# Performance work log

Hardware: AMD Instinct MI355X
Metric: run time of the kernel (lower is better)

Reference implementation:

```python
import jax, jax.numpy as jnp
import numpy as np
from jax import lax

B, N, C, H = 1024, 169, 256, 4   # n must equal window**2 = 169
A, W = 169, 13                   # agent_num, window; pool_size = sqrt(A) = 13 = h
HD = C // H


def setup_inputs() -> dict:
    key = jax.random.key(0)
    ks = jax.random.split(key, 13)
    s = 0.02
    return {
        "x": jax.random.normal(ks[0], (B, N, C), jnp.float32),
        "qkv_w": jax.random.normal(ks[1], (3 * C, C), jnp.float32) * s,
        "proj_w": jax.random.normal(ks[2], (C, C), jnp.float32) * s,
        "proj_b": jnp.zeros((C,), jnp.float32),
        "dwc_w": jax.random.normal(ks[3], (C, 1, 3, 3), jnp.float32) * s,  # depthwise OIHW
        "dwc_b": jnp.zeros((C,), jnp.float32),
        "an_bias": jax.random.normal(ks[4], (H, A, 13, 13), jnp.float32) * s,
        "na_bias": jax.random.normal(ks[5], (H, A, 13, 13), jnp.float32) * s,
        "ah_bias": jax.random.normal(ks[6], (1, H, A, W, 1), jnp.float32) * s,
        "aw_bias": jax.random.normal(ks[7], (1, H, A, 1, W), jnp.float32) * s,
        "ha_bias": jax.random.normal(ks[8], (1, H, W, 1, A), jnp.float32) * s,
        "wa_bias": jax.random.normal(ks[9], (1, H, 1, W, A), jnp.float32) * s,
    }


def reference(x, qkv_w, proj_w, proj_b, dwc_w, dwc_b,
              an_bias, na_bias, ah_bias, aw_bias, ha_bias, wa_bias):
    b, n, c = x.shape
    h = w = int(n ** 0.5)           # 13
    scale = HD ** (-0.5)

    qkv = (x @ qkv_w.T).reshape(b, n, 3, c)   # (b,n,3,c)
    q, k, v = qkv[:, :, 0], qkv[:, :, 1], qkv[:, :, 2]

    # AdaptiveAvgPool2d to (sqrt(A), sqrt(A)) = (13,13) == (h,w): identity pooling
    agent = q  # (b, A, c) since A == n here

    q4 = q.reshape(b, n, H, HD).transpose(0, 2, 1, 3)       # (b,H,n,hd)
    k4 = k.reshape(b, n, H, HD).transpose(0, 2, 1, 3)
    v4 = v.reshape(b, n, H, HD).transpose(0, 2, 1, 3)
    a4 = agent.reshape(b, A, H, HD).transpose(0, 2, 1, 3)   # (b,H,A,hd)

    # bilinear interp of 13x13 bias to (window,window)=(13,13) is identity
    pos_bias = an_bias.reshape(1, H, A, W * W) \
             + (ah_bias + aw_bias).reshape(1, H, A, W * W)   # (1,H,A,n)

    agent_attn = jax.nn.softmax(
        scale * jnp.einsum('bhad,bhnd->bhan', a4, k4) + pos_bias, axis=-1)
    agent_v = jnp.einsum('bhan,bhnd->bhad', agent_attn, v4)  # (b,H,A,hd)

    agent_bias = na_bias.reshape(1, H, A, W * W).transpose(0, 1, 3, 2) \
               + (ha_bias + wa_bias).reshape(1, H, W * W, A)  # (1,H,n,A)

    q_attn = jax.nn.softmax(
        scale * jnp.einsum('bhnd,bhad->bhna', q4, a4) + agent_bias, axis=-1)
    out = jnp.einsum('bhna,bhad->bhnd', q_attn, agent_v)     # (b,H,n,hd)
    out = out.transpose(0, 2, 1, 3).reshape(b, n, c)

    # depthwise 3x3 conv on v (NCHW), residual add
    v_img = v4.transpose(0, 2, 1, 3).reshape(b, h, w, c).transpose(0, 3, 1, 2)
    dw = lax.conv_general_dilated(
        v_img, dwc_w, (1, 1), ((1, 1), (1, 1)),
        feature_group_count=c,
        dimension_numbers=('NCHW', 'OIHW', 'NCHW')) + dwc_b[None, :, None, None]
    out = out + dw.transpose(0, 2, 3, 1).reshape(b, n, c)

    return out @ proj_w.T + proj_b
```

## Files before the change

### kernel.cpp

```cpp
#include <hip/hip_runtime.h>


typedef __attribute__((ext_vector_type(8))) short bf16x8;
typedef __attribute__((ext_vector_type(4))) float f32x4;

#define BSTR  67584
#define OFF_Q 0
#define OFF_K 22528
#define OFF_V 45056
#define OFF_T 135168
#define SMEM_BYTES 162816
#define WS_NEED 1307168ull

__device__ __forceinline__ unsigned short f2bf(float f) {
  unsigned int u = __float_as_uint(f);
  u += 0x7FFFu + ((u >> 16) & 1u);
  return (unsigned short)(u >> 16);
}
__device__ __forceinline__ float bf2f(unsigned short v) {
  return __uint_as_float(((unsigned int)v) << 16);
}
__device__ __forceinline__ f32x4 mfma16(bf16x8 a, bf16x8 b, f32x4 c) {
  return __builtin_amdgcn_mfma_f32_16x16x32_bf16(a, b, c, 0, 0, 0);
}
__device__ __forceinline__ bf16x8 cvt8(float4 a, float4 b) {
  bf16x8 v;
  v[0] = (short)f2bf(a.x); v[1] = (short)f2bf(a.y);
  v[2] = (short)f2bf(a.z); v[3] = (short)f2bf(a.w);
  v[4] = (short)f2bf(b.x); v[5] = (short)f2bf(b.y);
  v[6] = (short)f2bf(b.z); v[7] = (short)f2bf(b.w);
  return v;
}
__device__ __forceinline__ bf16x8 ld8s(const char* sm, int base, int stride, int row, int colbyte) {
  return *(const bf16x8*)(sm + base + row * stride + (colbyte ^ ((row & 7) << 4)));
}
__device__ __forceinline__ void st2s(char* sm, int base, int stride, int row, int col, unsigned short v) {
  *(unsigned short*)(sm + base + row * stride + ((col * 2) ^ ((row & 7) << 4))) = v;
}
__device__ __forceinline__ bf16x8 ld8p(const char* sm, int base, int stride, int row, int colbyte) {
  return *(const bf16x8*)(sm + base + row * stride + colbyte);
}
__device__ __forceinline__ void st2p(char* sm, int base, int stride, int row, int col, unsigned short v) {
  *(unsigned short*)(sm + base + row * stride + col * 2) = v;
}
__device__ __forceinline__ float ld2p(const char* sm, int base, int stride, int row, int col) {
  return bf2f(*(const unsigned short*)(sm + base + row * stride + col * 2));
}

__global__ void prep_kernel(
    const float* __restrict__ qkv_w,
    const float* __restrict__ an, const float* __restrict__ ah,
    const float* __restrict__ aw, const float* __restrict__ na,
    const float* __restrict__ ha, const float* __restrict__ wa,
    float* __restrict__ pos1, float* __restrict__ abias,
    unsigned short* __restrict__ qkvb)
{
  const int i = blockIdx.x * 256 + threadIdx.x;
  if (i < 114244) {
    const int hh = i / 28561;
    const int rem = i - hh * 28561;
    const int a = rem / 169;
    const int n = rem - a * 169;
    const int y = n / 13;
    const int xx = n - y * 13;
    pos1[i] = an[i] + ah[(hh * 169 + a) * 13 + y] + aw[(hh * 169 + a) * 13 + xx];
  } else if (i < 228488) {
    const int j = i - 114244;
    const int hh = j / 28561;
    const int rem = j - hh * 28561;
    const int n = rem / 169;
    const int a = rem - n * 169;
    const int y = n / 13;
    const int xx = n - y * 13;
    abias[j] = na[(hh * 169 + a) * 169 + n] + ha[(hh * 13 + y) * 169 + a]
             + wa[(hh * 13 + xx) * 169 + a];
  } else if (i < 425096) {
    const int k = i - 228488;
    qkvb[k] = f2bf(qkv_w[k]);
  }
}

template<int USEWS>
__global__ __launch_bounds__(768) void attn_kernel(
    const float* __restrict__ x, const float* __restrict__ qkv_w,
    const float* __restrict__ dwc_w, const float* __restrict__ dwc_b,
    const float* __restrict__ an, const float* __restrict__ ah,
    const float* __restrict__ aw, const float* __restrict__ na,
    const float* __restrict__ ha, const float* __restrict__ wa,
    const float* __restrict__ pos1, const float* __restrict__ abias,
    const unsigned short* __restrict__ qkvb,
    float* __restrict__ out)
{
  __shared__ __align__(16) char sm[SMEM_BYTES];
  const int tid = threadIdx.x;
  const int wave = tid >> 6;
  const int lane = tid & 63;
  const int l15 = lane & 15;
  const int l4 = lane >> 4;
  const int mt = wave;
  const f32x4 z = {0.f, 0.f, 0.f, 0.f};

  const float* xbp[2];
  float* op[2];
  xbp[0] = x + (size_t)blockIdx.x * 43264;
  xbp[1] = x + (size_t)(blockIdx.x + 512) * 43264;
  op[0] = out + (size_t)blockIdx.x * 43264;
  op[1] = out + (size_t)(blockIdx.x + 512) * 43264;

  {
    int* p = (int*)sm;
    for (int i = tid; i < SMEM_BYTES / 4; i += 768) p[i] = 0;
  }

  auto fused = [&](int sOff, int pvOff, int which, int h, f32x4 (&o)[2][4]) {
#pragma unroll
    for (int bb = 0; bb < 2; ++bb)
#pragma unroll
      for (int dt = 0; dt < 4; ++dt) o[bb][dt] = z;
    if (mt >= 11) return;
    const int arow = mt * 16 + l15;
    const int rbase = mt * 16 + l4 * 4;
    bf16x8 a0[2], a1[2];
#pragma unroll
    for (int bb = 0; bb < 2; ++bb) {
      a0[bb] = ld8s(sm, bb * BSTR + OFF_Q, 128, arow, l4 * 16);
      a1[bb] = ld8s(sm, bb * BSTR + OFF_Q, 128, arow, 64 + l4 * 16);
    }
    f32x4 s[2][11];
#pragma unroll
    for (int nt = 0; nt < 11; ++nt) {
      const int brow = nt * 16 + l15;
#pragma unroll
      for (int bb = 0; bb < 2; ++bb) {
        bf16x8 b0 = ld8s(sm, bb * BSTR + sOff, 128, brow, l4 * 16);
        bf16x8 b1 = ld8s(sm, bb * BSTR + sOff, 128, brow, 64 + l4 * 16);
        f32x4 c = z;
        c = mfma16(a0[bb], b0, c);
        c = mfma16(a1[bb], b1, c);
        s[bb][nt] = c;
      }
    }
    const float* bt = (which == 0) ? (pos1 + h * 28561) : (abias + h * 28561);
#pragma unroll
    for (int nt = 0; nt < 11; ++nt) {
      const int cc = nt * 16 + l15;
      const int ccl = cc > 168 ? 168 : cc;
      const int yc = (ccl * 79) >> 10;
      const int xc = ccl - yc * 13;
#pragma unroll
      for (int r = 0; r < 4; ++r) {
        const int rr = rbase + r;
        const int rrl = rr > 168 ? 168 : rr;
        float bias;
        if constexpr (USEWS) {
          bias = bt[rrl * 169 + ccl];
        } else {
          if (which == 0) {
            bias = an[h * 28561 + rrl * 169 + ccl]
                 + ah[(h * 169 + rrl) * 13 + yc]
                 + aw[(h * 169 + rrl) * 13 + xc];
          } else {
            const int yn = (rrl * 79) >> 10;
            const int xn = rrl - yn * 13;
            bias = na[h * 28561 + ccl * 169 + rrl]
                 + ha[(h * 13 + yn) * 169 + ccl]
                 + wa[(h * 13 + xn) * 169 + ccl];
          }
        }
#pragma unroll
        for (int bb = 0; bb < 2; ++bb) {
          const float v = s[bb][nt][r] * 0.125f + bias;
          s[bb][nt][r] = (cc > 168) ? -3.0e38f : v;
        }
      }
    }
#pragma unroll
    for (int bb = 0; bb < 2; ++bb)
#pragma unroll
      for (int r = 0; r < 4; ++r) {
        float m = s[bb][0][r];
#pragma unroll
        for (int nt = 1; nt < 11; ++nt) m = fmaxf(m, s[bb][nt][r]);
        m = fmaxf(m, __shfl_xor(m, 1));
        m = fmaxf(m, __shfl_xor(m, 2));
        m = fmaxf(m, __shfl_xor(m, 4));
        m = fmaxf(m, __shfl_xor(m, 8));
        float sum = 0.f;
#pragma unroll
        for (int nt = 0; nt < 11; ++nt) { const float e = __expf(s[bb][nt][r] - m); s[bb][nt][r] = e; sum += e; }
        sum += __shfl_xor(sum, 1);
        sum += __shfl_xor(sum, 2);
        sum += __shfl_xor(sum, 4);
        sum += __shfl_xor(sum, 8);
        const float inv = 1.f / sum;
#pragma unroll
        for (int nt = 0; nt < 11; ++nt) s[bb][nt][r] *= inv;
      }
#pragma unroll
    for (int np = 0; np < 6; ++np) {
      const int nt1 = 2 * np + 1;
      bf16x8 af[2];
#pragma unroll
      for (int bb = 0; bb < 2; ++bb) {
        const int tb = OFF_T + (wave * 2 + bb) * 1152;
#pragma unroll
        for (int r = 0; r < 4; ++r) {
          char* prow = sm + tb + (l4 * 4 + r) * 72;
          *(unsigned short*)(prow + l15 * 2) = f2bf(s[bb][2 * np][r]);
          *(unsigned short*)(prow + 32 + l15 * 2) =
              (nt1 < 11) ? f2bf(s[bb][nt1][r]) : (unsigned short)0;
        }
        af[bb] = *(const bf16x8*)(sm + tb + l15 * 72 + l4 * 16);
      }
#pragma unroll
      for (int dt = 0; dt < 4; ++dt)
#pragma unroll
        for (int bb = 0; bb < 2; ++bb) {
          bf16x8 bv = ld8p(sm, bb * BSTR + pvOff, 352, dt * 16 + l15, np * 64 + l4 * 16);
          o[bb][dt] = mfma16(af[bb], bv, o[bb][dt]);
        }
    }
  };

  for (int h = 0; h < 4; ++h) {
    __syncthreads();

    if (mt < 11) {
      f32x4 acc[2][12];
#pragma unroll
      for (int bb = 0; bb < 2; ++bb)
#pragma unroll
        for (int i = 0; i < 12; ++i) acc[bb][i] = z;
      const int arow = mt * 16 + l15;
      const int gr = arow < 169 ? arow : 168;

      for (int ks = 0; ks < 8; ++ks) {
        bf16x8 af[2];
#pragma unroll
        for (int bb = 0; bb < 2; ++bb) {
          const float* p0 = xbp[bb] + gr * 256 + ks * 32 + l4 * 8;
          af[bb] = cvt8(*(const float4*)p0, *(const float4*)(p0 + 4));
        }
#pragma unroll
        for (int nt = 0; nt < 12; ++nt) {
          const int wrow = nt * 16 + l15;
          const int grow = ((wrow >> 6) << 8) + h * 64 + (wrow & 63);
          bf16x8 bw;
          if constexpr (USEWS) {
            bw = *(const bf16x8*)(qkvb + (size_t)grow * 256 + ks * 32 + l4 * 8);
          } else {
            const float* wp = qkv_w + grow * 256 + ks * 32 + l4 * 8;
            bw = cvt8(*(const float4*)wp, *(const float4*)(wp + 4));
          }
          acc[0][nt] = mfma16(af[0], bw, acc[0][nt]);
          acc[1][nt] = mfma16(af[1], bw, acc[1][nt]);
        }
      }
#pragma unroll
      for (int nt = 0; nt < 12; ++nt) {
        const int mat = nt >> 2;
        const int d = (nt & 3) * 16 + l15;
#pragma unroll
        for (int r = 0; r < 4; ++r) {
          const int n = mt * 16 + l4 * 4 + r;
#pragma unroll
          for (int bb = 0; bb < 2; ++bb) {
            const unsigned short u = f2bf(acc[bb][nt][r]);
            if (mat == 0)      st2s(sm, bb * BSTR + OFF_Q, 128, n, d, u);
            else if (mat == 1) st2s(sm, bb * BSTR + OFF_K, 128, n, d, u);
            else               st2p(sm, bb * BSTR + OFF_V, 352, d, n, u);
          }
        }
      }
    }
    __syncthreads();

    f32x4 o1[2][4];
    fused(OFF_K, OFF_V, 0, h, o1);
    __syncthreads();
    if (mt < 11) {
#pragma unroll
      for (int bb = 0; bb < 2; ++bb)
#pragma unroll
        for (int dt = 0; dt < 4; ++dt)
#pragma unroll
          for (int r = 0; r < 4; ++r)
            st2p(sm, bb * BSTR + OFF_K, 352, dt * 16 + l15, mt * 16 + l4 * 4 + r,
                 f2bf(o1[bb][dt][r]));
    }
    __syncthreads();

    f32x4 o2[2][4];
    fused(OFF_Q, OFF_K, 1, h, o2);
    if (mt < 11) {
#pragma unroll
      for (int dt = 0; dt < 4; ++dt) {
        const int d = dt * 16 + l15;
        const int c = h * 64 + d;
        const float bc = dwc_b[c];
#pragma unroll
        for (int r = 0; r < 4; ++r) {
          const int n = mt * 16 + l4 * 4 + r;
          const int nl = n > 168 ? 168 : n;
          const int y = (nl * 79) >> 10;
          const int xx = nl - y * 13;
          float dw0 = bc, dw1 = bc;
#pragma unroll
          for (int ky = 0; ky < 3; ++ky) {
            const int yy = y + ky - 1;
            if ((unsigned)yy >= 13u) continue;
#pragma unroll
            for (int kx = 0; kx < 3; ++kx) {
              const int x2 = xx + kx - 1;
              if ((unsigned)x2 >= 13u) continue;
              const float wv = dwc_w[c * 9 + ky * 3 + kx];
              dw0 += wv * ld2p(sm, 0 * BSTR + OFF_V, 352, d, yy * 13 + x2);
              dw1 += wv * ld2p(sm, 1 * BSTR + OFF_V, 352, d, yy * 13 + x2);
            }
          }
          if (n < 169) {
            __builtin_nontemporal_store(o2[0][dt][r] + dw0, op[0] + (size_t)n * 256 + c);
            __builtin_nontemporal_store(o2[1][dt][r] + dw1, op[1] + (size_t)n * 256 + c);
          }
        }
      }
    }
  }
}

__global__ __launch_bounds__(512, 1) void proj_kernel(
    const float* __restrict__ pwf, const float* __restrict__ pb,
    float* __restrict__ out)
{
  __shared__ __align__(16) char sm[30720];
  const int bm = blockIdx.x;
  const int tid = threadIdx.x;
  const int wave = tid >> 6;
  const int lane = tid & 63;
  const int l15 = lane & 15;
  const int l4 = lane >> 4;
  const int wr = (wave >> 2) * 64;
  const int wc = (wave & 3) * 64;

  f32x4 acc[4][4];
  const f32x4 z = {0.f, 0.f, 0.f, 0.f};
#pragma unroll
  for (int i = 0; i < 4; ++i)
#pragma unroll
    for (int j = 0; j < 4; ++j) acc[i][j] = z;

  const int arow = tid >> 1, ahalf = tid & 1;
  const int brow = tid >> 1, bhalf = tid & 1;
  const float* asrc = out + ((size_t)bm * 128 + arow) * 256 + ahalf * 16;
  const float* bsrc = pwf + (size_t)brow * 256 + bhalf * 16;

  for (int kit = 0; kit < 8; ++kit) {
    const int k0 = kit * 32;
    bf16x8 aA0, aA1, aB0, aB1;
    if (tid < 256) {
      float4 f0 = *(const float4*)(asrc + k0);
      float4 f1 = *(const float4*)(asrc + k0 + 4);
      float4 f2 = *(const float4*)(asrc + k0 + 8);
      float4 f3 = *(const float4*)(asrc + k0 + 12);
      aA0 = cvt8(f0, f1); aA1 = cvt8(f2, f3);
    }
    {
      float4 f0 = *(const float4*)(bsrc + k0);
      float4 f1 = *(const float4*)(bsrc + k0 + 4);
      float4 f2 = *(const float4*)(bsrc + k0 + 8);
      float4 f3 = *(const float4*)(bsrc + k0 + 12);
      aB0 = cvt8(f0, f1); aB1 = cvt8(f2, f3);
    }
    __syncthreads();
    if (tid < 256) {
      *(bf16x8*)(sm + arow * 80 + ahalf * 32) = aA0;
      *(bf16x8*)(sm + arow * 80 + ahalf * 32 + 16) = aA1;
    }
    *(bf16x8*)(sm + 10240 + brow * 80 + bhalf * 32) = aB0;
    *(bf16x8*)(sm + 10240 + brow * 80 + bhalf * 32 + 16) = aB1;
    __syncthreads();
    bf16x8 afr[4], bfr[4];
#pragma unroll
    for (int mt = 0; mt < 4; ++mt)
      afr[mt] = *(const bf16x8*)(sm + (wr + mt * 16 + l15) * 80 + l4 * 16);
#pragma unroll
    for (int nt = 0; nt < 4; ++nt)
      bfr[nt] = *(const bf16x8*)(sm + 10240 + (wc + nt * 16 + l15) * 80 + l4 * 16);
#pragma unroll
    for (int mt = 0; mt < 4; ++mt)
#pragma unroll
      for (int nt = 0; nt < 4; ++nt)
        acc[mt][nt] = mfma16(afr[mt], bfr[nt], acc[mt][nt]);
  }
#pragma unroll
  for (int nt = 0; nt < 4; ++nt) {
    const int gcol = wc + nt * 16 + l15;
    const float bias = pb[gcol];
#pragma unroll
    for (int mt = 0; mt < 4; ++mt)
#pragma unroll
      for (int r = 0; r < 4; ++r) {
        const size_t grow = (size_t)bm * 128 + wr + mt * 16 + l4 * 4 + r;
        out[grow * 256 + gcol] = acc[mt][nt][r] + bias;
      }
  }
}

extern "C" void kernel_launch(void* const* d_in, const int* in_sizes, int n_in,
                              void* d_out, int out_size, void* d_ws, size_t ws_size,
                              hipStream_t stream) {
  const float* x      = (const float*)d_in[0];
  const float* qkv_w  = (const float*)d_in[1];
  const float* proj_w = (const float*)d_in[2];
  const float* proj_b = (const float*)d_in[3];
  const float* dwc_w  = (const float*)d_in[4];
  const float* dwc_b  = (const float*)d_in[5];
  const float* an     = (const float*)d_in[6];
  const float* na     = (const float*)d_in[7];
  const float* ah     = (const float*)d_in[8];
  const float* aw     = (const float*)d_in[9];
  const float* ha     = (const float*)d_in[10];
  const float* wa     = (const float*)d_in[11];
  float* outp = (float*)d_out;

  const bool usews = (d_ws != nullptr) && (ws_size >= WS_NEED);
  if (usews) {
    char* ws = (char*)d_ws;
    float* pos1  = (float*)ws;
    float* abias = (float*)(ws + 456976);
    unsigned short* qkvb = (unsigned short*)(ws + 913952);
    prep_kernel<<<1661, 256, 0, stream>>>(qkv_w, an, ah, aw, na, ha, wa,
                                          pos1, abias, qkvb);
    attn_kernel<1><<<512, 768, 0, stream>>>(
        x, qkv_w, dwc_w, dwc_b, an, ah, aw, na, ha, wa,
        pos1, abias, qkvb, outp);
  } else {
    attn_kernel<0><<<512, 768, 0, stream>>>(
        x, qkv_w, dwc_w, dwc_b, an, ah, aw, na, ha, wa,
        nullptr, nullptr, nullptr, outp);
  }
  proj_kernel<<<1352, 512, 0, stream>>>(proj_w, proj_b, outp);
}
```

Measured before the change: 1.065 ms.

## Pre-convert x to bf16 and swizzle V/agent-V shared layout

Adds a prep kernel that converts the whole input x to bf16 in workspace, so the QKV projection in the attention kernel loads bf16 directly instead of fp32 followed by in-loop conversion. The V and agent-V shared-memory tiles switch from padded stride 352 to an XOR-swizzled stride 384 to cut bank conflicts. The P-transpose staging buffer is shared across both batch items to save LDS. The extra pass reads x in fp32 and writes a bf16 copy, so it costs more total traffic than it saves in the attention kernel's reads, and it needs about 90 MB of workspace; without that, the old paths are used.

```diff
diff --git a/kernel.cpp b/kernel.cpp
--- a/kernel.cpp
+++ b/kernel.cpp
@@ -4,13 +4,14 @@
 typedef __attribute__((ext_vector_type(8))) short bf16x8;
 typedef __attribute__((ext_vector_type(4))) float f32x4;
 
-#define BSTR  67584
+#define BSTR  71680
 #define OFF_Q 0
 #define OFF_K 22528
-#define OFF_V 45056
-#define OFF_T 135168
-#define SMEM_BYTES 162816
-#define WS_NEED 1307168ull
+#define OFF_V 47104
+#define OFF_T 143360
+#define SMEM_BYTES 157184
+#define WS1 1307168ull
+#define WS2 89911840ull
 
 __device__ __forceinline__ unsigned short f2bf(float f) {
   unsigned int u = __float_as_uint(f);
@@ -37,14 +38,8 @@
 __device__ __forceinline__ void st2s(char* sm, int base, int stride, int row, int col, unsigned short v) {
   *(unsigned short*)(sm + base + row * stride + ((col * 2) ^ ((row & 7) << 4))) = v;
 }
-__device__ __forceinline__ bf16x8 ld8p(const char* sm, int base, int stride, int row, int colbyte) {
-  return *(const bf16x8*)(sm + base + row * stride + colbyte);
-}
-__device__ __forceinline__ void st2p(char* sm, int base, int stride, int row, int col, unsigned short v) {
-  *(unsigned short*)(sm + base + row * stride + col * 2) = v;
-}
-__device__ __forceinline__ float ld2p(const char* sm, int base, int stride, int row, int col) {
-  return bf2f(*(const unsigned short*)(sm + base + row * stride + col * 2));
+__device__ __forceinline__ float ld2s(const char* sm, int base, int stride, int row, int col) {
+  return bf2f(*(const unsigned short*)(sm + base + row * stride + ((col * 2) ^ ((row & 7) << 4))));
 }
 
 __global__ void prep_kernel(
@@ -80,7 +75,17 @@
   }
 }
 
-template<int USEWS>
+__global__ void prep2_kernel(const float* __restrict__ x, unsigned short* __restrict__ xb16)
+{
+  const size_t i = ((size_t)blockIdx.x * 256 + threadIdx.x) * 8;
+  if (i < 44302336ull) {
+    float4 f0 = *(const float4*)(x + i);
+    float4 f1 = *(const float4*)(x + i + 4);
+    *(bf16x8*)(xb16 + i) = cvt8(f0, f1);
+  }
+}
+
+template<int WSLVL>
 __global__ __launch_bounds__(768) void attn_kernel(
     const float* __restrict__ x, const float* __restrict__ qkv_w,
     const float* __restrict__ dwc_w, const float* __restrict__ dwc_b,
@@ -88,7 +93,7 @@
     const float* __restrict__ aw, const float* __restrict__ na,
     const float* __restrict__ ha, const float* __restrict__ wa,
     const float* __restrict__ pos1, const float* __restrict__ abias,
-    const unsigned short* __restrict__ qkvb,
+    const unsigned short* __restrict__ qkvb, const unsigned short* __restrict__ xb16,
     float* __restrict__ out)
 {
   __shared__ __align__(16) char sm[SMEM_BYTES];
@@ -101,9 +106,12 @@
   const f32x4 z = {0.f, 0.f, 0.f, 0.f};
 
   const float* xbp[2];
+  const unsigned short* xhp[2];
   float* op[2];
   xbp[0] = x + (size_t)blockIdx.x * 43264;
   xbp[1] = x + (size_t)(blockIdx.x + 512) * 43264;
+  xhp[0] = xb16 + (size_t)blockIdx.x * 43264;
+  xhp[1] = xb16 + (size_t)(blockIdx.x + 512) * 43264;
   op[0] = out + (size_t)blockIdx.x * 43264;
   op[1] = out + (size_t)(blockIdx.x + 512) * 43264;
 
@@ -152,7 +160,7 @@
         const int rr = rbase + r;
         const int rrl = rr > 168 ? 168 : rr;
         float bias;
-        if constexpr (USEWS) {
+        if constexpr (WSLVL >= 1) {
           bias = bt[rrl * 169 + ccl];
         } else {
           if (which == 0) {
@@ -196,13 +204,12 @@
 #pragma unroll
         for (int nt = 0; nt < 11; ++nt) s[bb][nt][r] *= inv;
       }
+    const int tb = OFF_T + wave * 1152;
 #pragma unroll
     for (int np = 0; np < 6; ++np) {
       const int nt1 = 2 * np + 1;
-      bf16x8 af[2];
 #pragma unroll
       for (int bb = 0; bb < 2; ++bb) {
-        const int tb = OFF_T + (wave * 2 + bb) * 1152;
 #pragma unroll
         for (int r = 0; r < 4; ++r) {
           char* prow = sm + tb + (l4 * 4 + r) * 72;
@@ -210,15 +217,13 @@
           *(unsigned short*)(prow + 32 + l15 * 2) =
               (nt1 < 11) ? f2bf(s[bb][nt1][r]) : (unsigned short)0;
         }
-        af[bb] = *(const bf16x8*)(sm + tb + l15 * 72 + l4 * 16);
-      }
-#pragma unroll
-      for (int dt = 0; dt < 4; ++dt)
-#pragma unroll
-        for (int bb = 0; bb < 2; ++bb) {
-          bf16x8 bv = ld8p(sm, bb * BSTR + pvOff, 352, dt * 16 + l15, np * 64 + l4 * 16);
-          o[bb][dt] = mfma16(af[bb], bv, o[bb][dt]);
-        }
+        bf16x8 af = *(const bf16x8*)(sm + tb + l15 * 72 + l4 * 16);
+#pragma unroll
+        for (int dt = 0; dt < 4; ++dt) {
+          bf16x8 bv = ld8s(sm, bb * BSTR + pvOff, 384, dt * 16 + l15, np * 64 + l4 * 16);
+          o[bb][dt] = mfma16(af, bv, o[bb][dt]);
+        }
+      }
     }
   };
 
@@ -238,15 +243,19 @@
         bf16x8 af[2];
 #pragma unroll
         for (int bb = 0; bb < 2; ++bb) {
-          const float* p0 = xbp[bb] + gr * 256 + ks * 32 + l4 * 8;
-          af[bb] = cvt8(*(const float4*)p0, *(const float4*)(p0 + 4));
+          if constexpr (WSLVL == 2) {
+            af[bb] = *(const bf16x8*)(xhp[bb] + gr * 256 + ks * 32 + l4 * 8);
+          } else {
+            const float* p0 = xbp[bb] + gr * 256 + ks * 32 + l4 * 8;
+            af[bb] = cvt8(*(const float4*)p0, *(const float4*)(p0 + 4));
+          }
         }
 #pragma unroll
         for (int nt = 0; nt < 12; ++nt) {
           const int wrow = nt * 16 + l15;
           const int grow = ((wrow >> 6) << 8) + h * 64 + (wrow & 63);
           bf16x8 bw;
-          if constexpr (USEWS) {
+          if constexpr (WSLVL >= 1) {
             bw = *(const bf16x8*)(qkvb + (size_t)grow * 256 + ks * 32 + l4 * 8);
           } else {
             const float* wp = qkv_w + grow * 256 + ks * 32 + l4 * 8;
@@ -268,7 +277,7 @@
             const unsigned short u = f2bf(acc[bb][nt][r]);
             if (mat == 0)      st2s(sm, bb * BSTR + OFF_Q, 128, n, d, u);
             else if (mat == 1) st2s(sm, bb * BSTR + OFF_K, 128, n, d, u);
-            else               st2p(sm, bb * BSTR + OFF_V, 352, d, n, u);
+            else               st2s(sm, bb * BSTR + OFF_V, 384, d, n, u);
           }
         }
       }
@@ -285,7 +294,7 @@
         for (int dt = 0; dt < 4; ++dt)
 #pragma unroll
           for (int r = 0; r < 4; ++r)
-            st2p(sm, bb * BSTR + OFF_K, 352, dt * 16 + l15, mt * 16 + l4 * 4 + r,
+            st2s(sm, bb * BSTR + OFF_K, 384, dt * 16 + l15, mt * 16 + l4 * 4 + r,
                  f2bf(o1[bb][dt][r]));
     }
     __syncthreads();
@@ -314,8 +323,8 @@
               const int x2 = xx + kx - 1;
               if ((unsigned)x2 >= 13u) continue;
               const float wv = dwc_w[c * 9 + ky * 3 + kx];
-              dw0 += wv * ld2p(sm, 0 * BSTR + OFF_V, 352, d, yy * 13 + x2);
-              dw1 += wv * ld2p(sm, 1 * BSTR + OFF_V, 352, d, yy * 13 + x2);
+              dw0 += wv * ld2s(sm, 0 * BSTR + OFF_V, 384, d, yy * 13 + x2);
+              dw1 += wv * ld2s(sm, 1 * BSTR + OFF_V, 384, d, yy * 13 + x2);
             }
           }
           if (n < 169) {
@@ -423,21 +432,24 @@
   const float* wa     = (const float*)d_in[11];
   float* outp = (float*)d_out;
 
-  const bool usews = (d_ws != nullptr) && (ws_size >= WS_NEED);
-  if (usews) {
-    char* ws = (char*)d_ws;
-    float* pos1  = (float*)ws;
-    float* abias = (float*)(ws + 456976);
-    unsigned short* qkvb = (unsigned short*)(ws + 913952);
-    prep_kernel<<<1661, 256, 0, stream>>>(qkv_w, an, ah, aw, na, ha, wa,
-                                          pos1, abias, qkvb);
+  char* ws = (char*)d_ws;
+  float* pos1  = (float*)ws;
+  float* abias = (float*)(ws + 456976);
+  unsigned short* qkvb = (unsigned short*)(ws + 913952);
+  unsigned short* xb16 = (unsigned short*)(ws + 1307168);
+
+  if (d_ws != nullptr && ws_size >= WS2) {
+    prep_kernel<<<1661, 256, 0, stream>>>(qkv_w, an, ah, aw, na, ha, wa, pos1, abias, qkvb);
+    prep2_kernel<<<21632, 256, 0, stream>>>(x, xb16);
+    attn_kernel<2><<<512, 768, 0, stream>>>(
+        x, qkv_w, dwc_w, dwc_b, an, ah, aw, na, ha, wa, pos1, abias, qkvb, xb16, outp);
+  } else if (d_ws != nullptr && ws_size >= WS1) {
+    prep_kernel<<<1661, 256, 0, stream>>>(qkv_w, an, ah, aw, na, ha, wa, pos1, abias, qkvb);
     attn_kernel<1><<<512, 768, 0, stream>>>(
-        x, qkv_w, dwc_w, dwc_b, an, ah, aw, na, ha, wa,
-        pos1, abias, qkvb, outp);
+        x, qkv_w, dwc_w, dwc_b, an, ah, aw, na, ha, wa, pos1, abias, qkvb, nullptr, outp);
   } else {
     attn_kernel<0><<<512, 768, 0, stream>>>(
-        x, qkv_w, dwc_w, dwc_b, an, ah, aw, na, ha, wa,
-        nullptr, nullptr, nullptr, outp);
+        x, qkv_w, dwc_w, dwc_b, an, ah, aw, na, ha, wa, nullptr, nullptr, nullptr, nullptr, outp);
   }
   proj_kernel<<<1352, 512, 0, stream>>>(proj_w, proj_b, outp);
 }
```

New measurement: 1.162 ms. 1.09x slower.
